# Performance work log

Measured on AMD Instinct MI355X. Metric: run time of the kernel, lower is better.

The kernel has to match this reference:

```python
import jax, jax.numpy as jnp
import numpy as np

B, N = 16, 512          # graphs, nodes per graph (equal-size dynamic batch)
IN, HID, OUT, K = 256, 128, 256, 16  # hidden = in_dim // red_factor
EPS = 1e-5


def setup_inputs() -> dict:
    key = jax.random.key(0)
    ks = jax.random.split(key, 12)
    def lin(k, fi, fo):
        return jax.random.normal(k, (fi, fo), jnp.float32) / np.sqrt(fi).astype(np.float32)
    return {
        "obj_encs": jax.random.normal(ks[0], (B * N, IN), jnp.float32),
        "n_nodes": jnp.full((B,), N, dtype=jnp.int32),
        # self-graph-attention params (in -> hidden), with residual projection
        "Wq": lin(ks[1], IN, HID), "bq": jnp.zeros((HID,), jnp.float32),
        "Wk": lin(ks[2], IN, HID), "bk": jnp.zeros((HID,), jnp.float32),
        "Wv": lin(ks[3], IN, HID), "bv": jnp.zeros((HID,), jnp.float32),
        "Wr": lin(ks[4], IN, HID), "br": jnp.zeros((HID,), jnp.float32),
        # EdgeConv (local+global => 2*HID input features)
        "Wc": lin(ks[5], 2 * HID, OUT), "bc": jnp.zeros((OUT,), jnp.float32),
        # LayerNorm affine
        "ln_scale": jnp.ones((OUT,), jnp.float32),
        "ln_bias": jnp.zeros((OUT,), jnp.float32),
    }


def _forward(obj_encs, n_nodes, Wq, bq, Wk, bk, Wv, bv, Wr, br, Wc, bc, ln_scale, ln_bias):
    # dynamic batching: equal-size graphs per n_nodes -> reshape [B, N, IN]
    x = obj_encs.reshape(B, N, IN)

    # --- SelfGraphAttentionLinear (per-graph dot-product attention, residual) ---
    q = x @ Wq + bq                      # [B, N, HID]
    kk = x @ Wk + bk
    v = x @ Wv + bv
    attn = jax.nn.softmax(jnp.einsum('bnd,bmd->bnm', q, kk) / np.sqrt(HID).astype(np.float32), axis=-1)
    h = jnp.einsum('bnm,bmd->bnd', attn, v) + (x @ Wr + br)  # residual projection

    # --- GraphConv: kNN (euclidean) within each graph ---
    sq = jnp.sum(h * h, axis=-1)                             # [B, N]
    dist = sq[:, :, None] + sq[:, None, :] - 2.0 * jnp.einsum('bnd,bmd->bnm', h, h)
    _, idx = jax.lax.top_k(-dist, K)                         # [B, N, K] (self included)

    nb = jax.vmap(lambda hb, ib: hb[ib])(h, idx)             # [B, N, K, HID]
    hc = h[:, :, None, :]                                    # [B, N, 1, HID]
    # features='local+global': [x_i, x_j - x_i]
    e = jnp.concatenate([jnp.broadcast_to(hc, nb.shape), nb - hc], axis=-1)  # [B,N,K,2H]

    y = jnp.einsum('bnkf,fo->bnko', e, Wc) + bc              # [B, N, K, OUT]
    y = jnp.max(y, axis=2)                                   # reduction='max' over k

    mu = jnp.mean(y, axis=-1, keepdims=True)
    var = jnp.mean((y - mu) ** 2, axis=-1, keepdims=True)
    y = (y - mu) / jnp.sqrt(var + EPS) * ln_scale + ln_bias  # LayerNorm
    return jax.nn.selu(y).reshape(B * N, OUT)


def reference(obj_encs, n_nodes, Wq, bq, Wk, bk, Wv, bv, Wr, br, Wc, bc, ln_scale, ln_bias):
    return _forward(obj_encs, n_nodes, Wq, bq, Wk, bk, Wv, bv, Wr, br, Wc, bc, ln_scale, ln_bias)
```

## Files before the change

### kernel.cpp

```cpp
#include <hip/hip_runtime.h>
#include <math.h>

#define NB   16
#define NN   512
#define FIN  256
#define HID  128
#define FOUT 256
#define TOPK 16
#define ROWS (NB*NN)
#define LN_EPS 1e-5f

#define BK   32
#define LDK  40
#define NTHR 256

typedef __attribute__((ext_vector_type(8)))  short  bf16x8;
typedef __attribute__((ext_vector_type(4)))  float  f32x4;
typedef __attribute__((ext_vector_type(8)))  unsigned short u16x8;

#define MFMA3(d, ah, al, bh, bl)                                              \
    d = __builtin_amdgcn_mfma_f32_16x16x32_bf16(ah, bh, d, 0, 0, 0);          \
    d = __builtin_amdgcn_mfma_f32_16x16x32_bf16(ah, bl, d, 0, 0, 0);          \
    d = __builtin_amdgcn_mfma_f32_16x16x32_bf16(al, bh, d, 0, 0, 0);

__device__ __forceinline__ ushort f2bf_rn(float x) {
    uint u = __float_as_uint(x);
    u += 0x7fff + ((u >> 16) & 1);
    return (ushort)(u >> 16);
}
__device__ __forceinline__ float bf2f(ushort h) {
    return __uint_as_float(((uint)h) << 16);
}
__device__ __forceinline__ void split2(float x, ushort& hi, ushort& lo) {
    hi = f2bf_rn(x);
    lo = f2bf_rn(x - bf2f(hi));
}

__device__ __forceinline__ void stage_rows64f(ushort (*Dh)[LDK], ushort (*Dl)[LDK],
                                              const float* __restrict__ src,
                                              int rstride, int tid)
{
    const int r = tid >> 2, seg = (tid & 3) * 8;
    const float* p = src + (size_t)r * rstride + seg;
    #pragma unroll
    for (int i = 0; i < 2; i++) {
        const float4 q = *(const float4*)(p + 4*i);
        ushort h0,l0,h1,l1,h2,l2,h3,l3;
        split2(q.x,h0,l0); split2(q.y,h1,l1);
        split2(q.z,h2,l2); split2(q.w,h3,l3);
        *(ushort4*)&Dh[r][seg + 4*i] = make_ushort4(h0,h1,h2,h3);
        *(ushort4*)&Dl[r][seg + 4*i] = make_ushort4(l0,l1,l2,l3);
    }
}

__device__ __forceinline__ void stage_cols64f(ushort (*Dh)[LDK], ushort (*Dl)[LDK],
                                              const float* __restrict__ src,
                                              int ldn, int tid)
{
    const int n = tid & 63, kh = (tid >> 6) * 8;
    const float* p = src + (size_t)kh * ldn + n;
    ushort hh[8], ll[8];
    #pragma unroll
    for (int i = 0; i < 8; i++) split2(p[(size_t)i * ldn], hh[i], ll[i]);
    *(ushort4*)&Dh[n][kh]     = make_ushort4(hh[0],hh[1],hh[2],hh[3]);
    *(ushort4*)&Dh[n][kh + 4] = make_ushort4(hh[4],hh[5],hh[6],hh[7]);
    *(ushort4*)&Dl[n][kh]     = make_ushort4(ll[0],ll[1],ll[2],ll[3]);
    *(ushort4*)&Dl[n][kh + 4] = make_ushort4(ll[4],ll[5],ll[6],ll[7]);
}

__device__ __forceinline__ void stage_u(ushort (*Ds)[LDK], const ushort* __restrict__ src,
                                        int rstride, int tid)
{
    const int r = tid >> 2, seg = (tid & 3) * 8;
    *(u16x8*)&Ds[r][seg] = *(const u16x8*)(src + (size_t)r * rstride + seg);
}

__device__ __forceinline__ void mma_step64(const ushort (*Ah)[LDK], const ushort (*Al)[LDK],
                                           const ushort (*Bh)[LDK], const ushort (*Bl)[LDK],
                                           f32x4 acc[2][2], int wr, int wc, int lane)
{
    const int q8 = (lane >> 4) * 8, m = lane & 15;
    bf16x8 ah[2], al[2], bh[2], bl[2];
    #pragma unroll
    for (int i = 0; i < 2; i++) {
        ah[i] = *(const bf16x8*)&Ah[wr + 16*i + m][q8];
        al[i] = *(const bf16x8*)&Al[wr + 16*i + m][q8];
        bh[i] = *(const bf16x8*)&Bh[wc + 16*i + m][q8];
        bl[i] = *(const bf16x8*)&Bl[wc + 16*i + m][q8];
    }
    #pragma unroll
    for (int i = 0; i < 2; i++)
        #pragma unroll
        for (int j = 0; j < 2; j++) {
            MFMA3(acc[i][j], ah[i], al[i], bh[j], bl[j]);
        }
}

struct Params {
    const float *X, *Wq, *bq, *Wk, *bk, *Wv, *bv, *Wr, *br, *Wc, *bc, *lns, *lnb;
    float *out;
    float *Rbuf, *SQ, *AB, *D, *Opart, *Mpart, *Lpart;
    ushort *Yh, *Yl, *Vth, *Vtl, *Hh, *Hl;
};

__device__ void phaseA(const Params& P, ushort* SMEM, int blk, int nblk)
{
    ushort (*Ah)[LDK] = (ushort(*)[LDK])(SMEM);
    ushort (*Al)[LDK] = (ushort(*)[LDK])(SMEM + 2560);
    ushort (*Bh)[LDK] = (ushort(*)[LDK])(SMEM + 5120);
    ushort (*Bl)[LDK] = (ushort(*)[LDK])(SMEM + 7680);
    float* fbuf = (float*)SMEM;

    const int tid = threadIdx.x, lane = tid & 63, w = tid >> 6;
    const int wr = (w >> 1) * 32, wc = (w & 1) * 32;
    const int m = lane & 15, q4 = (lane >> 4) * 4;

    for (int job = blk; job < 1024; job += nblk) {
        const int ct = job >> 7, br0 = (job & 127) * 64;
        const int widx = ct >> 1, ch = (ct & 1) * 64;
        const float* W    = widx==0 ? P.Wq : widx==1 ? P.Wk : widx==2 ? P.Wv : P.Wr;
        const float* bias = widx==0 ? P.bq : widx==1 ? P.bk : widx==2 ? P.bv : P.br;
        __syncthreads();
        f32x4 acc[2][2];
        #pragma unroll
        for (int i = 0; i < 2; i++)
            #pragma unroll
            for (int j = 0; j < 2; j++) acc[i][j] = (f32x4){0.f,0.f,0.f,0.f};

        for (int k0 = 0; k0 < FIN; k0 += BK) {
            stage_rows64f(Ah, Al, P.X + (size_t)br0 * FIN + k0, FIN, tid);
            stage_cols64f(Bh, Bl, W + (size_t)k0 * HID + ch, HID, tid);
            __syncthreads();
            mma_step64(Ah, Al, Bh, Bl, acc, wr, wc, lane);
            __syncthreads();
        }
        #pragma unroll
        for (int i = 0; i < 2; i++)
            #pragma unroll
            for (int reg = 0; reg < 4; reg++) {
                const int r = wr + 16*i + q4 + reg;
                #pragma unroll
                for (int j = 0; j < 2; j++) {
                    const int c = wc + 16*j + m;
                    fbuf[r*65 + c] = acc[i][j][reg] + bias[ch + c];
                }
            }
        __syncthreads();

        if (ct < 4) {
            const int r = tid >> 2, cs = (tid & 3) * 16;
            u16x8 vh0, vh1, vl0, vl1;
            #pragma unroll
            for (int t = 0; t < 8; t++) {
                ushort hh, ll;
                split2(fbuf[r*65 + cs + t], hh, ll);     vh0[t]=hh; vl0[t]=ll;
                split2(fbuf[r*65 + cs + 8 + t], hh, ll); vh1[t]=hh; vl1[t]=ll;
            }
            const size_t o = (size_t)(br0 + r) * 256 + ct*64 + cs;
            *(u16x8*)&P.Yh[o]   = vh0; *(u16x8*)&P.Yh[o+8] = vh1;
            *(u16x8*)&P.Yl[o]   = vl0; *(u16x8*)&P.Yl[o+8] = vl1;
        } else if (ct < 6) {
            const int cl = tid >> 2, rs = (tid & 3) * 16;
            const int b = br0 >> 9, nb = br0 & 511;
            const int cglob = (ct - 4) * 64 + cl;
            u16x8 vh0, vh1, vl0, vl1;
            #pragma unroll
            for (int t = 0; t < 8; t++) {
                ushort hh, ll;
                split2(fbuf[(rs+t)*65 + cl], hh, ll);   vh0[t]=hh; vl0[t]=ll;
                split2(fbuf[(rs+8+t)*65 + cl], hh, ll); vh1[t]=hh; vl1[t]=ll;
            }
            const size_t o = ((size_t)b*128 + cglob) * 512 + nb + rs;
            *(u16x8*)&P.Vth[o]   = vh0; *(u16x8*)&P.Vth[o+8] = vh1;
            *(u16x8*)&P.Vtl[o]   = vl0; *(u16x8*)&P.Vtl[o+8] = vl1;
        } else {
            const int r = tid >> 2, cs = (tid & 3) * 16;
            float* dst = P.Rbuf + (size_t)(br0 + r) * 128 + (ct - 6)*64 + cs;
            #pragma unroll
            for (int t = 0; t < 16; t += 4) {
                float4 q;
                q.x = fbuf[r*65+cs+t];   q.y = fbuf[r*65+cs+t+1];
                q.z = fbuf[r*65+cs+t+2]; q.w = fbuf[r*65+cs+t+3];
                *(float4*)(dst + t) = q;
            }
        }
    }
}

__device__ void phaseB(const Params& P, ushort* SMEM, int blk, int nblk)
{
    ushort (*P0h)[LDK] = (ushort(*)[LDK])(SMEM);
    ushort (*P0l)[LDK] = (ushort(*)[LDK])(SMEM + 2560);
    ushort (*Bh)[LDK]  = (ushort(*)[LDK])(SMEM + 5120);
    ushort (*Bl)[LDK]  = (ushort(*)[LDK])(SMEM + 7680);

    const int tid = threadIdx.x, lane = tid & 63, w = tid >> 6;
    const int L = lane & 15, quad = lane >> 4;
    const float scale = 0.08838834764831845f;

    for (int job = blk; job < 1024; job += nblk) {
        const int b = job >> 6, rest = job & 63;
        const int n0 = (rest >> 3) * 64, mc = rest & 7, m0 = mc * 64;
        const int grow0 = b*NN + n0 + w*16;

        bf16x8 qh[4], ql[4];
        #pragma unroll
        for (int s = 0; s < 4; s++) {
            const size_t qo = (size_t)(grow0 + L) * 256 + s*32 + quad*8;
            qh[s] = *(const bf16x8*)(P.Yh + qo);
            ql[s] = *(const bf16x8*)(P.Yl + qo);
        }

        f32x4 Sf[4];
        #pragma unroll
        for (int j = 0; j < 4; j++) Sf[j] = (f32x4){0.f,0.f,0.f,0.f};

        for (int s = 0; s < 4; s++) {
            __syncthreads();
            {
                const int r = tid >> 2, seg = (tid & 3) * 8;
                const size_t o = (size_t)(b*NN + m0 + r) * 256 + 128 + s*32 + seg;
                *(u16x8*)&Bh[r][seg] = *(const u16x8*)(P.Yh + o);
                *(u16x8*)&Bl[r][seg] = *(const u16x8*)(P.Yl + o);
            }
            __syncthreads();
            #pragma unroll
            for (int j = 0; j < 4; j++) {
                bf16x8 kh = *(const bf16x8*)&Bh[16*j + L][quad*8];
                bf16x8 kl = *(const bf16x8*)&Bl[16*j + L][quad*8];
                MFMA3(Sf[j], qh[s], ql[s], kh, kl);
            }
        }
        #pragma unroll
        for (int j = 0; j < 4; j++)
            #pragma unroll
            for (int r = 0; r < 4; r++) Sf[j][r] *= scale;

        float mx[4], ls[4];
        #pragma unroll
        for (int r = 0; r < 4; r++) {
            float v = fmaxf(fmaxf(Sf[0][r], Sf[1][r]), fmaxf(Sf[2][r], Sf[3][r]));
            v = fmaxf(v, __shfl_xor(v, 1));
            v = fmaxf(v, __shfl_xor(v, 2));
            v = fmaxf(v, __shfl_xor(v, 4));
            v = fmaxf(v, __shfl_xor(v, 8));
            mx[r] = v; ls[r] = 0.f;
        }

        __syncthreads();

        #pragma unroll
        for (int j = 0; j < 4; j++)
            #pragma unroll
            for (int r = 0; r < 4; r++) {
                const float p = __expf(Sf[j][r] - mx[r]);
                ls[r] += p;
                const int row = w*16 + quad*4 + r, cc = (16*j + (lane & 15)) & 31;
                ushort hh, ll; split2(p, hh, ll);
                if (j < 2) { P0h[row][cc] = hh; P0l[row][cc] = ll; }
                else       { Bh[row][cc]  = hh; Bl[row][cc]  = ll; }
            }
        #pragma unroll
        for (int r = 0; r < 4; r++) {
            float v = ls[r];
            v += __shfl_xor(v, 1); v += __shfl_xor(v, 2);
            v += __shfl_xor(v, 4); v += __shfl_xor(v, 8);
            ls[r] = v;
        }

        f32x4 O[8];
        #pragma unroll
        for (int j = 0; j < 8; j++) O[j] = (f32x4){0.f,0.f,0.f,0.f};
        #pragma unroll
        for (int s2 = 0; s2 < 2; s2++) {
            bf16x8 ph = s2 ? *(const bf16x8*)&Bh[w*16 + L][quad*8]
                           : *(const bf16x8*)&P0h[w*16 + L][quad*8];
            bf16x8 pl = s2 ? *(const bf16x8*)&Bl[w*16 + L][quad*8]
                           : *(const bf16x8*)&P0l[w*16 + L][quad*8];
            #pragma unroll
            for (int j = 0; j < 8; j++) {
                const size_t vo = ((size_t)(b*128 + 16*j + L)) * 512 + m0 + s2*32 + quad*8;
                bf16x8 vh = *(const bf16x8*)(P.Vth + vo);
                bf16x8 vl = *(const bf16x8*)(P.Vtl + vo);
                MFMA3(O[j], ph, pl, vh, vl);
            }
        }

        #pragma unroll
        for (int j = 0; j < 8; j++)
            #pragma unroll
            for (int reg = 0; reg < 4; reg++) {
                const int grow = grow0 + quad*4 + reg;
                P.Opart[((size_t)mc*ROWS + grow)*128 + 16*j + L] = O[j][reg];
            }
        if (L == 0) {
            #pragma unroll
            for (int reg = 0; reg < 4; reg++) {
                const int grow = grow0 + quad*4 + reg;
                P.Mpart[(size_t)mc*ROWS + grow] = mx[reg];
                P.Lpart[(size_t)mc*ROWS + grow] = ls[reg];
            }
        }
    }
}

__device__ void phaseC(const Params& P, int blk, int nblk)
{
    const int lane = threadIdx.x & 63, w = threadIdx.x >> 6;
    for (int row = blk*4 + w; row < ROWS; row += nblk*4) {
        float mp[8], M = -INFINITY;
        #pragma unroll
        for (int p = 0; p < 8; p++) {
            mp[p] = P.Mpart[(size_t)p*ROWS + row];
            M = fmaxf(M, mp[p]);
        }
        float Ls = 0.f, o0 = 0.f, o1 = 0.f;
        #pragma unroll
        for (int p = 0; p < 8; p++) {
            const float e = __expf(mp[p] - M);
            Ls += e * P.Lpart[(size_t)p*ROWS + row];
            const float* op = P.Opart + ((size_t)p*ROWS + row)*128;
            o0 += e * op[lane];
            o1 += e * op[lane + 64];
        }
        const float invl = 1.0f / Ls;
        const float h0 = o0*invl + P.Rbuf[(size_t)row*128 + lane];
        const float h1 = o1*invl + P.Rbuf[(size_t)row*128 + lane + 64];
        ushort hh, ll;
        split2(h0, hh, ll); P.Hh[(size_t)row*128 + lane] = hh;      P.Hl[(size_t)row*128 + lane] = ll;
        split2(h1, hh, ll); P.Hh[(size_t)row*128 + lane + 64] = hh; P.Hl[(size_t)row*128 + lane + 64] = ll;
        float s = h0*h0 + h1*h1;
        #pragma unroll
        for (int off = 1; off < 64; off <<= 1) s += __shfl_xor(s, off);
        if (lane == 0) P.SQ[row] = s;
    }
}

__device__ void phaseD(const Params& P, ushort* SMEM, int blk, int nblk)
{
    ushort (*Ah)[LDK] = (ushort(*)[LDK])(SMEM);
    ushort (*Al)[LDK] = (ushort(*)[LDK])(SMEM + 2560);
    ushort (*Bh)[LDK] = (ushort(*)[LDK])(SMEM + 5120);
    ushort (*Bl)[LDK] = (ushort(*)[LDK])(SMEM + 7680);

    const int tid = threadIdx.x, lane = tid & 63, w = tid >> 6;
    const int wr = (w >> 1) * 32, wc = (w & 1) * 32;
    const int m = lane & 15, q4 = (lane >> 4) * 4;

    for (int job = blk; job < 2048; job += nblk) {
        __syncthreads();
        f32x4 acc[2][2];
        #pragma unroll
        for (int i = 0; i < 2; i++)
            #pragma unroll
            for (int j = 0; j < 2; j++) acc[i][j] = (f32x4){0.f,0.f,0.f,0.f};

        if (job < 1024) {
            const int ct = job >> 7, br0 = (job & 127) * 64;
            const bool bhalf = ct >= 4;
            const int c0 = (ct & 3) * 64;
            for (int k0 = 0; k0 < HID; k0 += BK) {
                stage_u(Ah, P.Hh + (size_t)br0 * 128 + k0, 128, tid);
                stage_u(Al, P.Hl + (size_t)br0 * 128 + k0, 128, tid);
                {
                    const int n = tid & 63, kh2 = (tid >> 6) * 8;
                    ushort hh[8], llv[8];
                    #pragma unroll
                    for (int i = 0; i < 8; i++) {
                        const int k = k0 + kh2 + i;
                        const float bot = P.Wc[(size_t)(HID + k) * FOUT + c0 + n];
                        const float val = bhalf ? bot
                                                : (P.Wc[(size_t)k * FOUT + c0 + n] - bot);
                        split2(val, hh[i], llv[i]);
                    }
                    *(ushort4*)&Bh[n][kh2]     = make_ushort4(hh[0],hh[1],hh[2],hh[3]);
                    *(ushort4*)&Bh[n][kh2 + 4] = make_ushort4(hh[4],hh[5],hh[6],hh[7]);
                    *(ushort4*)&Bl[n][kh2]     = make_ushort4(llv[0],llv[1],llv[2],llv[3]);
                    *(ushort4*)&Bl[n][kh2 + 4] = make_ushort4(llv[4],llv[5],llv[6],llv[7]);
                }
                __syncthreads();
                mma_step64(Ah, Al, Bh, Bl, acc, wr, wc, lane);
                __syncthreads();
            }
            #pragma unroll
            for (int i = 0; i < 2; i++)
                #pragma unroll
                for (int reg = 0; reg < 4; reg++) {
                    const int grow = br0 + wr + 16*i + q4 + reg;
                    #pragma unroll
                    for (int j = 0; j < 2; j++) {
                        const int c = wc + 16*j + m;
                        const float add = bhalf ? 0.0f : P.bc[c0 + c];
                        P.AB[(size_t)grow * 512 + ct*64 + c] = acc[i][j][reg] + add;
                    }
                }
        } else {
            const int t = job - 1024;
            const int b = t >> 6, rest = t & 63;
            const int m0 = (rest >> 3) * 64, n0 = (rest & 7) * 64;
            for (int k0 = 0; k0 < HID; k0 += BK) {
                stage_u(Ah, P.Hh + (size_t)(b*NN + n0) * 128 + k0, 128, tid);
                stage_u(Al, P.Hl + (size_t)(b*NN + n0) * 128 + k0, 128, tid);
                stage_u(Bh, P.Hh + (size_t)(b*NN + m0) * 128 + k0, 128, tid);
                stage_u(Bl, P.Hl + (size_t)(b*NN + m0) * 128 + k0, 128, tid);
                __syncthreads();
                mma_step64(Ah, Al, Bh, Bl, acc, wr, wc, lane);
                __syncthreads();
            }
            const int gb = b * NN;
            float* Db = P.D + (size_t)b * NN * NN;
            float sqm[2];
            #pragma unroll
            for (int j = 0; j < 2; j++) sqm[j] = P.SQ[gb + m0 + wc + 16*j + m];
            #pragma unroll
            for (int i = 0; i < 2; i++)
                #pragma unroll
                for (int reg = 0; reg < 4; reg++) {
                    const int n = n0 + wr + 16*i + q4 + reg;
                    const float sqn = P.SQ[gb + n];
                    #pragma unroll
                    for (int j = 0; j < 2; j++)
                        Db[(size_t)n * NN + m0 + wc + 16*j + m]
                            = sqn + sqm[j] - 2.0f * acc[i][j][reg];
                }
        }
    }
}

__device__ void phaseE(const Params& P, int blk, int nblk)
{
    const int lane = threadIdx.x & 63, w = threadIdx.x >> 6;
    for (int row = blk*4 + w; row < ROWS; row += nblk*4) {
        const int gb0 = row & ~(NN - 1);
        const float* drow = P.D + (size_t)row * NN;
        const float4 dq0 = ((const float4*)drow)[lane];
        const float4 dq1 = ((const float4*)drow)[64 + lane];
        float v[8] = {dq0.x, dq0.y, dq0.z, dq0.w, dq1.x, dq1.y, dq1.z, dq1.w};

        const float lsc0 = P.lns[lane],       lbi0 = P.lnb[lane];
        const float lsc1 = P.lns[lane + 64],  lbi1 = P.lnb[lane + 64];
        const float lsc2 = P.lns[lane + 128], lbi2 = P.lnb[lane + 128];
        const float lsc3 = P.lns[lane + 192], lbi3 = P.lnb[lane + 192];
        const float* arow = P.AB + (size_t)row * 512;
        const float a0 = arow[lane], a1 = arow[lane + 64],
                    a2 = arow[lane + 128], a3 = arow[lane + 192];

        float bm0 = -INFINITY, bm1 = -INFINITY, bm2 = -INFINITY, bm3 = -INFINITY;

        for (int it = 0; it < TOPK; it++) {
            float bestv = v[0]; int bestm = 4*lane;
            #pragma unroll
            for (int j = 1; j < 8; j++) {
                const int mm = (j >> 2)*256 + 4*lane + (j & 3);
                if (v[j] < bestv) { bestv = v[j]; bestm = mm; }
            }
            #pragma unroll
            for (int off = 1; off < 64; off <<= 1) {
                const float ov = __shfl_xor(bestv, off);
                const int   om = __shfl_xor(bestm, off);
                if (ov < bestv || (ov == bestv && om < bestm)) { bestv = ov; bestm = om; }
            }
            const float* brow = P.AB + (size_t)(gb0 + bestm) * 512 + 256;
            bm0 = fmaxf(bm0, brow[lane]);
            bm1 = fmaxf(bm1, brow[lane + 64]);
            bm2 = fmaxf(bm2, brow[lane + 128]);
            bm3 = fmaxf(bm3, brow[lane + 192]);
            if (((bestm >> 2) & 63) == lane) {
                const int jj = ((bestm >> 8) << 2) | (bestm & 3);
                #pragma unroll
                for (int j = 0; j < 8; j++) if (j == jj) v[j] = INFINITY;
            }
        }

        float y0 = a0 + bm0, y1 = a1 + bm1, y2 = a2 + bm2, y3 = a3 + bm3;
        float s = y0 + y1 + y2 + y3;
        #pragma unroll
        for (int off = 1; off < 64; off <<= 1) s += __shfl_xor(s, off);
        const float mu = s * (1.0f/256.0f);
        const float d0 = y0 - mu, d1 = y1 - mu, d2 = y2 - mu, d3 = y3 - mu;
        float s2 = d0*d0 + d1*d1 + d2*d2 + d3*d3;
        #pragma unroll
        for (int off = 1; off < 64; off <<= 1) s2 += __shfl_xor(s2, off);
        const float var = s2 * (1.0f/256.0f);
        const float rstd = rsqrtf(var + LN_EPS);

        const float lam = 1.0507009873554805f, alpha = 1.6732632423543772f;
        float* orow = P.out + (size_t)row * FOUT;
        { const float z = d0*rstd*lsc0 + lbi0; orow[lane]       = z > 0.f ? lam*z : lam*alpha*expm1f(z); }
        { const float z = d1*rstd*lsc1 + lbi1; orow[lane + 64]  = z > 0.f ? lam*z : lam*alpha*expm1f(z); }
        { const float z = d2*rstd*lsc2 + lbi2; orow[lane + 128] = z > 0.f ? lam*z : lam*alpha*expm1f(z); }
        { const float z = d3*rstd*lsc3 + lbi3; orow[lane + 192] = z > 0.f ? lam*z : lam*alpha*expm1f(z); }
    }
}

__global__ __launch_bounds__(NTHR, 2) void k_pA(Params P) {
    __shared__ ushort SMEM[4*64*LDK];
    phaseA(P, SMEM, blockIdx.x, gridDim.x);
}
__global__ __launch_bounds__(NTHR, 2) void k_pB(Params P) {
    __shared__ ushort SMEM[4*64*LDK];
    phaseB(P, SMEM, blockIdx.x, gridDim.x);
}
__global__ __launch_bounds__(NTHR, 2) void k_pC(Params P) { phaseC(P, blockIdx.x, gridDim.x); }
__global__ __launch_bounds__(NTHR, 2) void k_pD(Params P) {
    __shared__ ushort SMEM[4*64*LDK];
    phaseD(P, SMEM, blockIdx.x, gridDim.x);
}
__global__ __launch_bounds__(NTHR, 2) void k_pE(Params P) { phaseE(P, blockIdx.x, gridDim.x); }

extern "C" void kernel_launch(void* const* d_in, const int* in_sizes, int n_in,
                              void* d_out, int out_size, void* d_ws, size_t ws_size,
                              hipStream_t stream)
{
    (void)in_sizes; (void)n_in; (void)out_size; (void)ws_size;

    char* cur = (char*)d_ws;
    auto alloc = [&](size_t bytes) { char* p = cur; cur += (bytes + 255) & ~size_t(255); return p; };

    Params P;
    P.X   = (const float*)d_in[0];
    P.Wq  = (const float*)d_in[2];
    P.bq  = (const float*)d_in[3];
    P.Wk  = (const float*)d_in[4];
    P.bk  = (const float*)d_in[5];
    P.Wv  = (const float*)d_in[6];
    P.bv  = (const float*)d_in[7];
    P.Wr  = (const float*)d_in[8];
    P.br  = (const float*)d_in[9];
    P.Wc  = (const float*)d_in[10];
    P.bc  = (const float*)d_in[11];
    P.lns = (const float*)d_in[12];
    P.lnb = (const float*)d_in[13];
    P.out = (float*)d_out;

    P.D     = (float*)alloc((size_t)NB*NN*NN*4);
    P.AB    = (float*)alloc((size_t)ROWS*512*4);
    P.Opart = (float*)alloc((size_t)8*ROWS*128*4);
    P.Mpart = (float*)alloc((size_t)8*ROWS*4);
    P.Lpart = (float*)alloc((size_t)8*ROWS*4);
    P.Rbuf  = (float*)alloc((size_t)ROWS*128*4);
    P.SQ    = (float*)alloc((size_t)ROWS*4);
    P.Yh    = (ushort*)alloc((size_t)ROWS*256*2);
    P.Yl    = (ushort*)alloc((size_t)ROWS*256*2);
    P.Vth   = (ushort*)alloc((size_t)NB*128*512*2);
    P.Vtl   = (ushort*)alloc((size_t)NB*128*512*2);
    P.Hh    = (ushort*)alloc((size_t)ROWS*128*2);
    P.Hl    = (ushort*)alloc((size_t)ROWS*128*2);

    k_pA<<<1024, NTHR, 0, stream>>>(P);
    k_pB<<<1024, NTHR, 0, stream>>>(P);
    k_pC<<<2048, NTHR, 0, stream>>>(P);
    k_pD<<<2048, NTHR, 0, stream>>>(P);
    k_pE<<<2048, NTHR, 0, stream>>>(P);
}
```

Baseline: 184.7 us.

## Pre-split inputs and weights into bf16 hi/lo in a prep kernel

Adds a prep kernel that converts X once into bf16 hi/lo arrays and pre-transposes and splits the QKVR and EdgeConv weights, including a folded (Wtop - Wbot) form, plus concatenated biases. Phase A then stages pre-split bf16 tiles with vector loads instead of splitting floats and doing strided column loads on every tile, and each phase becomes a one-job-per-block kernel. This removes the split work that was repeated across the column tiles of the projection GEMM. The cost is an extra launch and extra global traffic to write and re-read the bf16 copies of X.

```diff
diff --git a/kernel.cpp b/kernel.cpp
--- a/kernel.cpp
+++ b/kernel.cpp
@@ -36,38 +36,6 @@
     lo = f2bf_rn(x - bf2f(hi));
 }
 
-__device__ __forceinline__ void stage_rows64f(ushort (*Dh)[LDK], ushort (*Dl)[LDK],
-                                              const float* __restrict__ src,
-                                              int rstride, int tid)
-{
-    const int r = tid >> 2, seg = (tid & 3) * 8;
-    const float* p = src + (size_t)r * rstride + seg;
-    #pragma unroll
-    for (int i = 0; i < 2; i++) {
-        const float4 q = *(const float4*)(p + 4*i);
-        ushort h0,l0,h1,l1,h2,l2,h3,l3;
-        split2(q.x,h0,l0); split2(q.y,h1,l1);
-        split2(q.z,h2,l2); split2(q.w,h3,l3);
-        *(ushort4*)&Dh[r][seg + 4*i] = make_ushort4(h0,h1,h2,h3);
-        *(ushort4*)&Dl[r][seg + 4*i] = make_ushort4(l0,l1,l2,l3);
-    }
-}
-
-__device__ __forceinline__ void stage_cols64f(ushort (*Dh)[LDK], ushort (*Dl)[LDK],
-                                              const float* __restrict__ src,
-                                              int ldn, int tid)
-{
-    const int n = tid & 63, kh = (tid >> 6) * 8;
-    const float* p = src + (size_t)kh * ldn + n;
-    ushort hh[8], ll[8];
-    #pragma unroll
-    for (int i = 0; i < 8; i++) split2(p[(size_t)i * ldn], hh[i], ll[i]);
-    *(ushort4*)&Dh[n][kh]     = make_ushort4(hh[0],hh[1],hh[2],hh[3]);
-    *(ushort4*)&Dh[n][kh + 4] = make_ushort4(hh[4],hh[5],hh[6],hh[7]);
-    *(ushort4*)&Dl[n][kh]     = make_ushort4(ll[0],ll[1],ll[2],ll[3]);
-    *(ushort4*)&Dl[n][kh + 4] = make_ushort4(ll[4],ll[5],ll[6],ll[7]);
-}
-
 __device__ __forceinline__ void stage_u(ushort (*Ds)[LDK], const ushort* __restrict__ src,
                                         int rstride, int tid)
 {
@@ -99,12 +67,110 @@
 struct Params {
     const float *X, *Wq, *bq, *Wk, *bk, *Wv, *bv, *Wr, *br, *Wc, *bc, *lns, *lnb;
     float *out;
-    float *Rbuf, *SQ, *AB, *D, *Opart, *Mpart, *Lpart;
-    ushort *Yh, *Yl, *Vth, *Vtl, *Hh, *Hl;
+    float *Rbuf, *SQ, *AB, *D, *Opart, *Mpart, *Lpart, *bcat, *bcab;
+    ushort *Xh, *Xl, *Yh, *Yl, *Vth, *Vtl, *Hh, *Hl, *Wth, *Wtl, *Wcth, *Wctl;
 };
 
-__device__ void phaseA(const Params& P, ushort* SMEM, int blk, int nblk)
-{
+__global__ __launch_bounds__(NTHR) void k_prep(Params P)
+{
+    const int blk = blockIdx.x, tid = threadIdx.x;
+    __shared__ float fb[64][65];
+
+    if (blk >= 17) {
+        const size_t base = ((size_t)(blk - 17) * 256 + tid) * 8;
+        const float4 a = *(const float4*)(P.X + base);
+        const float4 b = *(const float4*)(P.X + base + 4);
+        u16x8 vh, vl; ushort hh, ll;
+        split2(a.x,hh,ll); vh[0]=hh; vl[0]=ll;
+        split2(a.y,hh,ll); vh[1]=hh; vl[1]=ll;
+        split2(a.z,hh,ll); vh[2]=hh; vl[2]=ll;
+        split2(a.w,hh,ll); vh[3]=hh; vl[3]=ll;
+        split2(b.x,hh,ll); vh[4]=hh; vl[4]=ll;
+        split2(b.y,hh,ll); vh[5]=hh; vl[5]=ll;
+        split2(b.z,hh,ll); vh[6]=hh; vl[6]=ll;
+        split2(b.w,hh,ll); vh[7]=hh; vl[7]=ll;
+        *(u16x8*)(P.Xh + base) = vh;
+        *(u16x8*)(P.Xl + base) = vl;
+        return;
+    }
+
+    if (blk < 8) {
+        const int n0 = blk * 64;
+        const int widx = n0 >> 7;
+        const float* W = widx==0 ? P.Wq : widx==1 ? P.Wk : widx==2 ? P.Wv : P.Wr;
+        const int cbase = n0 & 127;
+        for (int kt = 0; kt < 4; kt++) {
+            const int k0 = kt * 64;
+            __syncthreads();
+            {
+                const int kk = tid >> 2, cs = (tid & 3) * 16;
+                #pragma unroll
+                for (int t = 0; t < 16; t += 4) {
+                    const float4 q = *(const float4*)&W[(size_t)(k0+kk)*HID + cbase + cs + t];
+                    fb[kk][cs+t]=q.x; fb[kk][cs+t+1]=q.y; fb[kk][cs+t+2]=q.z; fb[kk][cs+t+3]=q.w;
+                }
+            }
+            __syncthreads();
+            {
+                const int c = tid >> 2, ks = (tid & 3) * 16;
+                u16x8 vh0, vh1, vl0, vl1;
+                #pragma unroll
+                for (int t = 0; t < 8; t++) {
+                    ushort hh, ll;
+                    split2(fb[ks+t][c], hh, ll);   vh0[t]=hh; vl0[t]=ll;
+                    split2(fb[ks+8+t][c], hh, ll); vh1[t]=hh; vl1[t]=ll;
+                }
+                *(u16x8*)&P.Wth[(size_t)(n0+c)*256 + k0 + ks]     = vh0;
+                *(u16x8*)&P.Wth[(size_t)(n0+c)*256 + k0 + ks + 8] = vh1;
+                *(u16x8*)&P.Wtl[(size_t)(n0+c)*256 + k0 + ks]     = vl0;
+                *(u16x8*)&P.Wtl[(size_t)(n0+c)*256 + k0 + ks + 8] = vl1;
+            }
+        }
+    } else if (blk < 16) {
+        const int n0 = (blk - 8) * 64;
+        const bool ahalf = n0 < 256;
+        const int cbase = n0 & 255;
+        for (int kt = 0; kt < 2; kt++) {
+            const int k0 = kt * 64;
+            __syncthreads();
+            {
+                const int kk = tid >> 2, cs = (tid & 3) * 16;
+                #pragma unroll
+                for (int t = 0; t < 16; t++) {
+                    const float bot = P.Wc[(size_t)(HID + k0 + kk)*FOUT + cbase + cs + t];
+                    float val = bot;
+                    if (ahalf) val = P.Wc[(size_t)(k0 + kk)*FOUT + cbase + cs + t] - bot;
+                    fb[kk][cs+t] = val;
+                }
+            }
+            __syncthreads();
+            {
+                const int c = tid >> 2, ks = (tid & 3) * 16;
+                u16x8 vh0, vh1, vl0, vl1;
+                #pragma unroll
+                for (int t = 0; t < 8; t++) {
+                    ushort hh, ll;
+                    split2(fb[ks+t][c], hh, ll);   vh0[t]=hh; vl0[t]=ll;
+                    split2(fb[ks+8+t][c], hh, ll); vh1[t]=hh; vl1[t]=ll;
+                }
+                *(u16x8*)&P.Wcth[(size_t)(n0+c)*128 + k0 + ks]     = vh0;
+                *(u16x8*)&P.Wcth[(size_t)(n0+c)*128 + k0 + ks + 8] = vh1;
+                *(u16x8*)&P.Wctl[(size_t)(n0+c)*128 + k0 + ks]     = vl0;
+                *(u16x8*)&P.Wctl[(size_t)(n0+c)*128 + k0 + ks + 8] = vl1;
+            }
+        }
+    } else {
+        for (int i = tid; i < 512; i += 256) {
+            const int w = i >> 7, c = i & 127;
+            P.bcat[i] = w==0 ? P.bq[c] : w==1 ? P.bk[c] : w==2 ? P.bv[c] : P.br[c];
+            P.bcab[i] = i < 256 ? P.bc[i] : 0.f;
+        }
+    }
+}
+
+__global__ __launch_bounds__(NTHR, 2) void k_pA(Params P)
+{
+    __shared__ ushort SMEM[4*64*LDK];
     ushort (*Ah)[LDK] = (ushort(*)[LDK])(SMEM);
     ushort (*Al)[LDK] = (ushort(*)[LDK])(SMEM + 2560);
     ushort (*Bh)[LDK] = (ushort(*)[LDK])(SMEM + 5120);
@@ -115,80 +181,80 @@
     const int wr = (w >> 1) * 32, wc = (w & 1) * 32;
     const int m = lane & 15, q4 = (lane >> 4) * 4;
 
-    for (int job = blk; job < 1024; job += nblk) {
-        const int ct = job >> 7, br0 = (job & 127) * 64;
-        const int widx = ct >> 1, ch = (ct & 1) * 64;
-        const float* W    = widx==0 ? P.Wq : widx==1 ? P.Wk : widx==2 ? P.Wv : P.Wr;
-        const float* bias = widx==0 ? P.bq : widx==1 ? P.bk : widx==2 ? P.bv : P.br;
+    const int job = blockIdx.x;
+    const int ct = job >> 7, br0 = (job & 127) * 64;
+
+    f32x4 acc[2][2];
+    #pragma unroll
+    for (int i = 0; i < 2; i++)
+        #pragma unroll
+        for (int j = 0; j < 2; j++) acc[i][j] = (f32x4){0.f,0.f,0.f,0.f};
+
+    for (int k0 = 0; k0 < FIN; k0 += BK) {
+        stage_u(Ah, P.Xh + (size_t)br0 * 256 + k0, 256, tid);
+        stage_u(Al, P.Xl + (size_t)br0 * 256 + k0, 256, tid);
+        stage_u(Bh, P.Wth + (size_t)(ct*64) * 256 + k0, 256, tid);
+        stage_u(Bl, P.Wtl + (size_t)(ct*64) * 256 + k0, 256, tid);
         __syncthreads();
-        f32x4 acc[2][2];
-        #pragma unroll
-        for (int i = 0; i < 2; i++)
+        mma_step64(Ah, Al, Bh, Bl, acc, wr, wc, lane);
+        __syncthreads();
+    }
+
+    #pragma unroll
+    for (int i = 0; i < 2; i++)
+        #pragma unroll
+        for (int reg = 0; reg < 4; reg++) {
+            const int r = wr + 16*i + q4 + reg;
             #pragma unroll
-            for (int j = 0; j < 2; j++) acc[i][j] = (f32x4){0.f,0.f,0.f,0.f};
-
-        for (int k0 = 0; k0 < FIN; k0 += BK) {
-            stage_rows64f(Ah, Al, P.X + (size_t)br0 * FIN + k0, FIN, tid);
-            stage_cols64f(Bh, Bl, W + (size_t)k0 * HID + ch, HID, tid);
-            __syncthreads();
-            mma_step64(Ah, Al, Bh, Bl, acc, wr, wc, lane);
-            __syncthreads();
-        }
-        #pragma unroll
-        for (int i = 0; i < 2; i++)
-            #pragma unroll
-            for (int reg = 0; reg < 4; reg++) {
-                const int r = wr + 16*i + q4 + reg;
-                #pragma unroll
-                for (int j = 0; j < 2; j++) {
-                    const int c = wc + 16*j + m;
-                    fbuf[r*65 + c] = acc[i][j][reg] + bias[ch + c];
-                }
-            }
-        __syncthreads();
-
-        if (ct < 4) {
-            const int r = tid >> 2, cs = (tid & 3) * 16;
-            u16x8 vh0, vh1, vl0, vl1;
-            #pragma unroll
-            for (int t = 0; t < 8; t++) {
-                ushort hh, ll;
-                split2(fbuf[r*65 + cs + t], hh, ll);     vh0[t]=hh; vl0[t]=ll;
-                split2(fbuf[r*65 + cs + 8 + t], hh, ll); vh1[t]=hh; vl1[t]=ll;
-            }
-            const size_t o = (size_t)(br0 + r) * 256 + ct*64 + cs;
-            *(u16x8*)&P.Yh[o]   = vh0; *(u16x8*)&P.Yh[o+8] = vh1;
-            *(u16x8*)&P.Yl[o]   = vl0; *(u16x8*)&P.Yl[o+8] = vl1;
-        } else if (ct < 6) {
-            const int cl = tid >> 2, rs = (tid & 3) * 16;
-            const int b = br0 >> 9, nb = br0 & 511;
-            const int cglob = (ct - 4) * 64 + cl;
-            u16x8 vh0, vh1, vl0, vl1;
-            #pragma unroll
-            for (int t = 0; t < 8; t++) {
-                ushort hh, ll;
-                split2(fbuf[(rs+t)*65 + cl], hh, ll);   vh0[t]=hh; vl0[t]=ll;
-                split2(fbuf[(rs+8+t)*65 + cl], hh, ll); vh1[t]=hh; vl1[t]=ll;
-            }
-            const size_t o = ((size_t)b*128 + cglob) * 512 + nb + rs;
-            *(u16x8*)&P.Vth[o]   = vh0; *(u16x8*)&P.Vth[o+8] = vh1;
-            *(u16x8*)&P.Vtl[o]   = vl0; *(u16x8*)&P.Vtl[o+8] = vl1;
-        } else {
-            const int r = tid >> 2, cs = (tid & 3) * 16;
-            float* dst = P.Rbuf + (size_t)(br0 + r) * 128 + (ct - 6)*64 + cs;
-            #pragma unroll
-            for (int t = 0; t < 16; t += 4) {
-                float4 q;
-                q.x = fbuf[r*65+cs+t];   q.y = fbuf[r*65+cs+t+1];
-                q.z = fbuf[r*65+cs+t+2]; q.w = fbuf[r*65+cs+t+3];
-                *(float4*)(dst + t) = q;
-            }
-        }
-    }
-}
-
-__device__ void phaseB(const Params& P, ushort* SMEM, int blk, int nblk)
-{
+            for (int j = 0; j < 2; j++) {
+                const int c = wc + 16*j + m;
+                fbuf[r*65 + c] = acc[i][j][reg] + P.bcat[ct*64 + c];
+            }
+        }
+    __syncthreads();
+
+    if (ct < 4) {
+        const int r = tid >> 2, cs = (tid & 3) * 16;
+        u16x8 vh0, vh1, vl0, vl1;
+        #pragma unroll
+        for (int t = 0; t < 8; t++) {
+            ushort hh, ll;
+            split2(fbuf[r*65 + cs + t], hh, ll);     vh0[t]=hh; vl0[t]=ll;
+            split2(fbuf[r*65 + cs + 8 + t], hh, ll); vh1[t]=hh; vl1[t]=ll;
+        }
+        const size_t o = (size_t)(br0 + r) * 256 + ct*64 + cs;
+        *(u16x8*)&P.Yh[o]   = vh0; *(u16x8*)&P.Yh[o+8] = vh1;
+        *(u16x8*)&P.Yl[o]   = vl0; *(u16x8*)&P.Yl[o+8] = vl1;
+    } else if (ct < 6) {
+        const int cl = tid >> 2, rs = (tid & 3) * 16;
+        const int b = br0 >> 9, nb = br0 & 511;
+        const int cglob = (ct - 4) * 64 + cl;
+        u16x8 vh0, vh1, vl0, vl1;
+        #pragma unroll
+        for (int t = 0; t < 8; t++) {
+            ushort hh, ll;
+            split2(fbuf[(rs+t)*65 + cl], hh, ll);   vh0[t]=hh; vl0[t]=ll;
+            split2(fbuf[(rs+8+t)*65 + cl], hh, ll); vh1[t]=hh; vl1[t]=ll;
+        }
+        const size_t o = ((size_t)b*128 + cglob) * 512 + nb + rs;
+        *(u16x8*)&P.Vth[o]   = vh0; *(u16x8*)&P.Vth[o+8] = vh1;
+        *(u16x8*)&P.Vtl[o]   = vl0; *(u16x8*)&P.Vtl[o+8] = vl1;
+    } else {
+        const int r = tid >> 2, cs = (tid & 3) * 16;
+        float* dst = P.Rbuf + (size_t)(br0 + r) * 128 + (ct - 6)*64 + cs;
+        #pragma unroll
+        for (int t = 0; t < 16; t += 4) {
+            float4 q;
+            q.x = fbuf[r*65+cs+t];   q.y = fbuf[r*65+cs+t+1];
+            q.z = fbuf[r*65+cs+t+2]; q.w = fbuf[r*65+cs+t+3];
+            *(float4*)(dst + t) = q;
+        }
+    }
+}
+
+__global__ __launch_bounds__(NTHR, 2) void k_pB(Params P)
+{
+    __shared__ ushort SMEM[4*64*LDK];
     ushort (*P0h)[LDK] = (ushort(*)[LDK])(SMEM);
     ushort (*P0l)[LDK] = (ushort(*)[LDK])(SMEM + 2560);
     ushort (*Bh)[LDK]  = (ushort(*)[LDK])(SMEM + 5120);
@@ -198,146 +264,145 @@
     const int L = lane & 15, quad = lane >> 4;
     const float scale = 0.08838834764831845f;
 
-    for (int job = blk; job < 1024; job += nblk) {
-        const int b = job >> 6, rest = job & 63;
-        const int n0 = (rest >> 3) * 64, mc = rest & 7, m0 = mc * 64;
-        const int grow0 = b*NN + n0 + w*16;
-
-        bf16x8 qh[4], ql[4];
-        #pragma unroll
-        for (int s = 0; s < 4; s++) {
-            const size_t qo = (size_t)(grow0 + L) * 256 + s*32 + quad*8;
-            qh[s] = *(const bf16x8*)(P.Yh + qo);
-            ql[s] = *(const bf16x8*)(P.Yl + qo);
-        }
-
-        f32x4 Sf[4];
-        #pragma unroll
-        for (int j = 0; j < 4; j++) Sf[j] = (f32x4){0.f,0.f,0.f,0.f};
-
-        for (int s = 0; s < 4; s++) {
-            __syncthreads();
-            {
-                const int r = tid >> 2, seg = (tid & 3) * 8;
-                const size_t o = (size_t)(b*NN + m0 + r) * 256 + 128 + s*32 + seg;
-                *(u16x8*)&Bh[r][seg] = *(const u16x8*)(P.Yh + o);
-                *(u16x8*)&Bl[r][seg] = *(const u16x8*)(P.Yl + o);
-            }
-            __syncthreads();
-            #pragma unroll
-            for (int j = 0; j < 4; j++) {
-                bf16x8 kh = *(const bf16x8*)&Bh[16*j + L][quad*8];
-                bf16x8 kl = *(const bf16x8*)&Bl[16*j + L][quad*8];
-                MFMA3(Sf[j], qh[s], ql[s], kh, kl);
-            }
-        }
-        #pragma unroll
-        for (int j = 0; j < 4; j++)
-            #pragma unroll
-            for (int r = 0; r < 4; r++) Sf[j][r] *= scale;
-
-        float mx[4], ls[4];
+    const int job = blockIdx.x;
+    const int b = job >> 6, rest = job & 63;
+    const int n0 = (rest >> 3) * 64, mc = rest & 7, m0 = mc * 64;
+    const int grow0 = b*NN + n0 + w*16;
+
+    bf16x8 qh[4], ql[4];
+    #pragma unroll
+    for (int s = 0; s < 4; s++) {
+        const size_t qo = (size_t)(grow0 + L) * 256 + s*32 + quad*8;
+        qh[s] = *(const bf16x8*)(P.Yh + qo);
+        ql[s] = *(const bf16x8*)(P.Yl + qo);
+    }
+
+    f32x4 Sf[4];
+    #pragma unroll
+    for (int j = 0; j < 4; j++) Sf[j] = (f32x4){0.f,0.f,0.f,0.f};
+
+    for (int s = 0; s < 4; s++) {
+        __syncthreads();
+        {
+            const int r = tid >> 2, seg = (tid & 3) * 8;
+            const size_t o = (size_t)(b*NN + m0 + r) * 256 + 128 + s*32 + seg;
+            *(u16x8*)&Bh[r][seg] = *(const u16x8*)(P.Yh + o);
+            *(u16x8*)&Bl[r][seg] = *(const u16x8*)(P.Yl + o);
+        }
+        __syncthreads();
+        #pragma unroll
+        for (int j = 0; j < 4; j++) {
+            bf16x8 kh = *(const bf16x8*)&Bh[16*j + L][quad*8];
+            bf16x8 kl = *(const bf16x8*)&Bl[16*j + L][quad*8];
+            MFMA3(Sf[j], qh[s], ql[s], kh, kl);
+        }
+    }
+    #pragma unroll
+    for (int j = 0; j < 4; j++)
+        #pragma unroll
+        for (int r = 0; r < 4; r++) Sf[j][r] *= scale;
+
+    float mx[4], ls[4];
+    #pragma unroll
+    for (int r = 0; r < 4; r++) {
+        float v = fmaxf(fmaxf(Sf[0][r], Sf[1][r]), fmaxf(Sf[2][r], Sf[3][r]));
+        v = fmaxf(v, __shfl_xor(v, 1));
+        v = fmaxf(v, __shfl_xor(v, 2));
+        v = fmaxf(v, __shfl_xor(v, 4));
+        v = fmaxf(v, __shfl_xor(v, 8));
+        mx[r] = v; ls[r] = 0.f;
+    }
+
+    __syncthreads();
+
+    #pragma unroll
+    for (int j = 0; j < 4; j++)
         #pragma unroll
         for (int r = 0; r < 4; r++) {
-            float v = fmaxf(fmaxf(Sf[0][r], Sf[1][r]), fmaxf(Sf[2][r], Sf[3][r]));
-            v = fmaxf(v, __shfl_xor(v, 1));
-            v = fmaxf(v, __shfl_xor(v, 2));
-            v = fmaxf(v, __shfl_xor(v, 4));
-            v = fmaxf(v, __shfl_xor(v, 8));
-            mx[r] = v; ls[r] = 0.f;
-        }
-
-        __syncthreads();
-
-        #pragma unroll
-        for (int j = 0; j < 4; j++)
-            #pragma unroll
-            for (int r = 0; r < 4; r++) {
-                const float p = __expf(Sf[j][r] - mx[r]);
-                ls[r] += p;
-                const int row = w*16 + quad*4 + r, cc = (16*j + (lane & 15)) & 31;
-                ushort hh, ll; split2(p, hh, ll);
-                if (j < 2) { P0h[row][cc] = hh; P0l[row][cc] = ll; }
-                else       { Bh[row][cc]  = hh; Bl[row][cc]  = ll; }
-            }
-        #pragma unroll
-        for (int r = 0; r < 4; r++) {
-            float v = ls[r];
-            v += __shfl_xor(v, 1); v += __shfl_xor(v, 2);
-            v += __shfl_xor(v, 4); v += __shfl_xor(v, 8);
-            ls[r] = v;
-        }
-
-        f32x4 O[8];
-        #pragma unroll
-        for (int j = 0; j < 8; j++) O[j] = (f32x4){0.f,0.f,0.f,0.f};
-        #pragma unroll
-        for (int s2 = 0; s2 < 2; s2++) {
-            bf16x8 ph = s2 ? *(const bf16x8*)&Bh[w*16 + L][quad*8]
-                           : *(const bf16x8*)&P0h[w*16 + L][quad*8];
-            bf16x8 pl = s2 ? *(const bf16x8*)&Bl[w*16 + L][quad*8]
-                           : *(const bf16x8*)&P0l[w*16 + L][quad*8];
-            #pragma unroll
-            for (int j = 0; j < 8; j++) {
-                const size_t vo = ((size_t)(b*128 + 16*j + L)) * 512 + m0 + s2*32 + quad*8;
-                bf16x8 vh = *(const bf16x8*)(P.Vth + vo);
-                bf16x8 vl = *(const bf16x8*)(P.Vtl + vo);
-                MFMA3(O[j], ph, pl, vh, vl);
-            }
-        }
-
-        #pragma unroll
-        for (int j = 0; j < 8; j++)
-            #pragma unroll
-            for (int reg = 0; reg < 4; reg++) {
-                const int grow = grow0 + quad*4 + reg;
-                P.Opart[((size_t)mc*ROWS + grow)*128 + 16*j + L] = O[j][reg];
-            }
-        if (L == 0) {
-            #pragma unroll
-            for (int reg = 0; reg < 4; reg++) {
-                const int grow = grow0 + quad*4 + reg;
-                P.Mpart[(size_t)mc*ROWS + grow] = mx[reg];
-                P.Lpart[(size_t)mc*ROWS + grow] = ls[reg];
-            }
-        }
-    }
-}
-
-__device__ void phaseC(const Params& P, int blk, int nblk)
+            const float p = __expf(Sf[j][r] - mx[r]);
+            ls[r] += p;
+            const int row = w*16 + quad*4 + r, cc = (16*j + L) & 31;
+            ushort hh, ll; split2(p, hh, ll);
+            if (j < 2) { P0h[row][cc] = hh; P0l[row][cc] = ll; }
+            else       { Bh[row][cc]  = hh; Bl[row][cc]  = ll; }
+        }
+    #pragma unroll
+    for (int r = 0; r < 4; r++) {
+        float v = ls[r];
+        v += __shfl_xor(v, 1); v += __shfl_xor(v, 2);
+        v += __shfl_xor(v, 4); v += __shfl_xor(v, 8);
+        ls[r] = v;
+    }
+
+    f32x4 O[8];
+    #pragma unroll
+    for (int j = 0; j < 8; j++) O[j] = (f32x4){0.f,0.f,0.f,0.f};
+    #pragma unroll
+    for (int s2 = 0; s2 < 2; s2++) {
+        bf16x8 ph = s2 ? *(const bf16x8*)&Bh[w*16 + L][quad*8]
+                       : *(const bf16x8*)&P0h[w*16 + L][quad*8];
+        bf16x8 pl = s2 ? *(const bf16x8*)&Bl[w*16 + L][quad*8]
+                       : *(const bf16x8*)&P0l[w*16 + L][quad*8];
+        #pragma unroll
+        for (int j = 0; j < 8; j++) {
+            const size_t vo = ((size_t)(b*128 + 16*j + L)) * 512 + m0 + s2*32 + quad*8;
+            bf16x8 vh = *(const bf16x8*)(P.Vth + vo);
+            bf16x8 vl = *(const bf16x8*)(P.Vtl + vo);
+            MFMA3(O[j], ph, pl, vh, vl);
+        }
+    }
+
+    #pragma unroll
+    for (int j = 0; j < 8; j++)
+        #pragma unroll
+        for (int reg = 0; reg < 4; reg++) {
+            const int grow = grow0 + quad*4 + reg;
+            P.Opart[((size_t)mc*ROWS + grow)*128 + 16*j + L] = O[j][reg];
+        }
+    if (L == 0) {
+        #pragma unroll
+        for (int reg = 0; reg < 4; reg++) {
+            const int grow = grow0 + quad*4 + reg;
+            P.Mpart[(size_t)mc*ROWS + grow] = mx[reg];
+            P.Lpart[(size_t)mc*ROWS + grow] = ls[reg];
+        }
+    }
+}
+
+__global__ __launch_bounds__(NTHR, 2) void k_pC(Params P)
 {
     const int lane = threadIdx.x & 63, w = threadIdx.x >> 6;
-    for (int row = blk*4 + w; row < ROWS; row += nblk*4) {
-        float mp[8], M = -INFINITY;
-        #pragma unroll
-        for (int p = 0; p < 8; p++) {
-            mp[p] = P.Mpart[(size_t)p*ROWS + row];
-            M = fmaxf(M, mp[p]);
-        }
-        float Ls = 0.f, o0 = 0.f, o1 = 0.f;
-        #pragma unroll
-        for (int p = 0; p < 8; p++) {
-            const float e = __expf(mp[p] - M);
-            Ls += e * P.Lpart[(size_t)p*ROWS + row];
-            const float* op = P.Opart + ((size_t)p*ROWS + row)*128;
-            o0 += e * op[lane];
-            o1 += e * op[lane + 64];
-        }
-        const float invl = 1.0f / Ls;
-        const float h0 = o0*invl + P.Rbuf[(size_t)row*128 + lane];
-        const float h1 = o1*invl + P.Rbuf[(size_t)row*128 + lane + 64];
-        ushort hh, ll;
-        split2(h0, hh, ll); P.Hh[(size_t)row*128 + lane] = hh;      P.Hl[(size_t)row*128 + lane] = ll;
-        split2(h1, hh, ll); P.Hh[(size_t)row*128 + lane + 64] = hh; P.Hl[(size_t)row*128 + lane + 64] = ll;
-        float s = h0*h0 + h1*h1;
-        #pragma unroll
-        for (int off = 1; off < 64; off <<= 1) s += __shfl_xor(s, off);
-        if (lane == 0) P.SQ[row] = s;
-    }
-}
-
-__device__ void phaseD(const Params& P, ushort* SMEM, int blk, int nblk)
-{
+    const int row = blockIdx.x * 4 + w;
+    float mp[8], M = -INFINITY;
+    #pragma unroll
+    for (int p = 0; p < 8; p++) {
+        mp[p] = P.Mpart[(size_t)p*ROWS + row];
+        M = fmaxf(M, mp[p]);
+    }
+    float Ls = 0.f, o0 = 0.f, o1 = 0.f;
+    #pragma unroll
+    for (int p = 0; p < 8; p++) {
+        const float e = __expf(mp[p] - M);
+        Ls += e * P.Lpart[(size_t)p*ROWS + row];
+        const float* op = P.Opart + ((size_t)p*ROWS + row)*128;
+        o0 += e * op[lane];
+        o1 += e * op[lane + 64];
+    }
+    const float invl = 1.0f / Ls;
+    const float h0 = o0*invl + P.Rbuf[(size_t)row*128 + lane];
+    const float h1 = o1*invl + P.Rbuf[(size_t)row*128 + lane + 64];
+    ushort hh, ll;
+    split2(h0, hh, ll); P.Hh[(size_t)row*128 + lane] = hh;      P.Hl[(size_t)row*128 + lane] = ll;
+    split2(h1, hh, ll); P.Hh[(size_t)row*128 + lane + 64] = hh; P.Hl[(size_t)row*128 + lane + 64] = ll;
+    float s = h0*h0 + h1*h1;
+    #pragma unroll
+    for (int off = 1; off < 64; off <<= 1) s += __shfl_xor(s, off);
+    if (lane == 0) P.SQ[row] = s;
+}
+
+__global__ __launch_bounds__(NTHR, 2) void k_pD(Params P)
+{
+    __shared__ ushort SMEM[4*64*LDK];
     ushort (*Ah)[LDK] = (ushort(*)[LDK])(SMEM);
     ushort (*Al)[LDK] = (ushort(*)[LDK])(SMEM + 2560);
     ushort (*Bh)[LDK] = (ushort(*)[LDK])(SMEM + 5120);
@@ -346,167 +411,132 @@
     const int tid = threadIdx.x, lane = tid & 63, w = tid >> 6;
     const int wr = (w >> 1) * 32, wc = (w & 1) * 32;
     const int m = lane & 15, q4 = (lane >> 4) * 4;
-
-    for (int job = blk; job < 2048; job += nblk) {
-        __syncthreads();
-        f32x4 acc[2][2];
+    const int job = blockIdx.x;
+
+    f32x4 acc[2][2];
+    #pragma unroll
+    for (int i = 0; i < 2; i++)
+        #pragma unroll
+        for (int j = 0; j < 2; j++) acc[i][j] = (f32x4){0.f,0.f,0.f,0.f};
+
+    if (job < 1024) {
+        const int ct = job >> 7, br0 = (job & 127) * 64;
+        for (int k0 = 0; k0 < HID; k0 += BK) {
+            stage_u(Ah, P.Hh + (size_t)br0 * 128 + k0, 128, tid);
+            stage_u(Al, P.Hl + (size_t)br0 * 128 + k0, 128, tid);
+            stage_u(Bh, P.Wcth + (size_t)(ct*64) * 128 + k0, 128, tid);
+            stage_u(Bl, P.Wctl + (size_t)(ct*64) * 128 + k0, 128, tid);
+            __syncthreads();
+            mma_step64(Ah, Al, Bh, Bl, acc, wr, wc, lane);
+            __syncthreads();
+        }
         #pragma unroll
         for (int i = 0; i < 2; i++)
             #pragma unroll
-            for (int j = 0; j < 2; j++) acc[i][j] = (f32x4){0.f,0.f,0.f,0.f};
-
-        if (job < 1024) {
-            const int ct = job >> 7, br0 = (job & 127) * 64;
-            const bool bhalf = ct >= 4;
-            const int c0 = (ct & 3) * 64;
-            for (int k0 = 0; k0 < HID; k0 += BK) {
-                stage_u(Ah, P.Hh + (size_t)br0 * 128 + k0, 128, tid);
-                stage_u(Al, P.Hl + (size_t)br0 * 128 + k0, 128, tid);
-                {
-                    const int n = tid & 63, kh2 = (tid >> 6) * 8;
-                    ushort hh[8], llv[8];
-                    #pragma unroll
-                    for (int i = 0; i < 8; i++) {
-                        const int k = k0 + kh2 + i;
-                        const float bot = P.Wc[(size_t)(HID + k) * FOUT + c0 + n];
-                        const float val = bhalf ? bot
-                                                : (P.Wc[(size_t)k * FOUT + c0 + n] - bot);
-                        split2(val, hh[i], llv[i]);
-                    }
-                    *(ushort4*)&Bh[n][kh2]     = make_ushort4(hh[0],hh[1],hh[2],hh[3]);
-                    *(ushort4*)&Bh[n][kh2 + 4] = make_ushort4(hh[4],hh[5],hh[6],hh[7]);
-                    *(ushort4*)&Bl[n][kh2]     = make_ushort4(llv[0],llv[1],llv[2],llv[3]);
-                    *(ushort4*)&Bl[n][kh2 + 4] = make_ushort4(llv[4],llv[5],llv[6],llv[7]);
+            for (int reg = 0; reg < 4; reg++) {
+                const int grow = br0 + wr + 16*i + q4 + reg;
+                #pragma unroll
+                for (int j = 0; j < 2; j++) {
+                    const int c = wc + 16*j + m;
+                    P.AB[(size_t)grow * 512 + ct*64 + c] = acc[i][j][reg] + P.bcab[ct*64 + c];
                 }
-                __syncthreads();
-                mma_step64(Ah, Al, Bh, Bl, acc, wr, wc, lane);
-                __syncthreads();
-            }
+            }
+    } else {
+        const int t = job - 1024;
+        const int b = t >> 6, rest = t & 63;
+        const int m0 = (rest >> 3) * 64, n0 = (rest & 7) * 64;
+        for (int k0 = 0; k0 < HID; k0 += BK) {
+            stage_u(Ah, P.Hh + (size_t)(b*NN + n0) * 128 + k0, 128, tid);
+            stage_u(Al, P.Hl + (size_t)(b*NN + n0) * 128 + k0, 128, tid);
+            stage_u(Bh, P.Hh + (size_t)(b*NN + m0) * 128 + k0, 128, tid);
+            stage_u(Bl, P.Hl + (size_t)(b*NN + m0) * 128 + k0, 128, tid);
+            __syncthreads();
+            mma_step64(Ah, Al, Bh, Bl, acc, wr, wc, lane);
+            __syncthreads();
+        }
+        const int gb = b * NN;
+        float* Db = P.D + (size_t)b * NN * NN;
+        float sqm[2];
+        #pragma unroll
+        for (int j = 0; j < 2; j++) sqm[j] = P.SQ[gb + m0 + wc + 16*j + m];
+        #pragma unroll
+        for (int i = 0; i < 2; i++)
             #pragma unroll
-            for (int i = 0; i < 2; i++)
+            for (int reg = 0; reg < 4; reg++) {
+                const int n = n0 + wr + 16*i + q4 + reg;
+                const float sqn = P.SQ[gb + n];
                 #pragma unroll
-                for (int reg = 0; reg < 4; reg++) {
-                    const int grow = br0 + wr + 16*i + q4 + reg;
-                    #pragma unroll
-                    for (int j = 0; j < 2; j++) {
-                        const int c = wc + 16*j + m;
-                        const float add = bhalf ? 0.0f : P.bc[c0 + c];
-                        P.AB[(size_t)grow * 512 + ct*64 + c] = acc[i][j][reg] + add;
-                    }
-                }
-        } else {
-            const int t = job - 1024;
-            const int b = t >> 6, rest = t & 63;
-            const int m0 = (rest >> 3) * 64, n0 = (rest & 7) * 64;
-            for (int k0 = 0; k0 < HID; k0 += BK) {
-                stage_u(Ah, P.Hh + (size_t)(b*NN + n0) * 128 + k0, 128, tid);
-                stage_u(Al, P.Hl + (size_t)(b*NN + n0) * 128 + k0, 128, tid);
-                stage_u(Bh, P.Hh + (size_t)(b*NN + m0) * 128 + k0, 128, tid);
-                stage_u(Bl, P.Hl + (size_t)(b*NN + m0) * 128 + k0, 128, tid);
-                __syncthreads();
-                mma_step64(Ah, Al, Bh, Bl, acc, wr, wc, lane);
-                __syncthreads();
-            }
-            const int gb = b * NN;
-            float* Db = P.D + (size_t)b * NN * NN;
-            float sqm[2];
+                for (int j = 0; j < 2; j++)
+                    Db[(size_t)n * NN + m0 + wc + 16*j + m]
+                        = sqn + sqm[j] - 2.0f * acc[i][j][reg];
+            }
+    }
+}
+
+__global__ __launch_bounds__(NTHR, 2) void k_pE(Params P)
+{
+    const int lane = threadIdx.x & 63, w = threadIdx.x >> 6;
+    const int row = blockIdx.x * 4 + w;
+    const int gb0 = row & ~(NN - 1);
+    const float* drow = P.D + (size_t)row * NN;
+    const float4 dq0 = ((const float4*)drow)[lane];
+    const float4 dq1 = ((const float4*)drow)[64 + lane];
+    float v[8] = {dq0.x, dq0.y, dq0.z, dq0.w, dq1.x, dq1.y, dq1.z, dq1.w};
+
+    const float lsc0 = P.lns[lane],       lbi0 = P.lnb[lane];
+    const float lsc1 = P.lns[lane + 64],  lbi1 = P.lnb[lane + 64];
+    const float lsc2 = P.lns[lane + 128], lbi2 = P.lnb[lane + 128];
+    const float lsc3 = P.lns[lane + 192], lbi3 = P.lnb[lane + 192];
+    const float* arow = P.AB + (size_t)row * 512;
+    const float a0 = arow[lane], a1 = arow[lane + 64],
+                a2 = arow[lane + 128], a3 = arow[lane + 192];
+
+    float bm0 = -INFINITY, bm1 = -INFINITY, bm2 = -INFINITY, bm3 = -INFINITY;
+
+    for (int it = 0; it < TOPK; it++) {
+        float bestv = v[0]; int bestm = 4*lane;
+        #pragma unroll
+        for (int j = 1; j < 8; j++) {
+            const int mm = (j >> 2)*256 + 4*lane + (j & 3);
+            if (v[j] < bestv) { bestv = v[j]; bestm = mm; }
+        }
+        #pragma unroll
+        for (int off = 1; off < 64; off <<= 1) {
+            const float ov = __shfl_xor(bestv, off);
+            const int   om = __shfl_xor(bestm, off);
+            if (ov < bestv || (ov == bestv && om < bestm)) { bestv = ov; bestm = om; }
+        }
+        const float* brow = P.AB + (size_t)(gb0 + bestm) * 512 + 256;
+        bm0 = fmaxf(bm0, brow[lane]);
+        bm1 = fmaxf(bm1, brow[lane + 64]);
+        bm2 = fmaxf(bm2, brow[lane + 128]);
+        bm3 = fmaxf(bm3, brow[lane + 192]);
+        if (((bestm >> 2) & 63) == lane) {
+            const int jj = ((bestm >> 8) << 2) | (bestm & 3);
             #pragma unroll
-            for (int j = 0; j < 2; j++) sqm[j] = P.SQ[gb + m0 + wc + 16*j + m];
-            #pragma unroll
-            for (int i = 0; i < 2; i++)
-                #pragma unroll
-                for (int reg = 0; reg < 4; reg++) {
-                    const int n = n0 + wr + 16*i + q4 + reg;
-                    const float sqn = P.SQ[gb + n];
-                    #pragma unroll
-                    for (int j = 0; j < 2; j++)
-                        Db[(size_t)n * NN + m0 + wc + 16*j + m]
-                            = sqn + sqm[j] - 2.0f * acc[i][j][reg];
-                }
-        }
-    }
-}
-
-__device__ void phaseE(const Params& P, int blk, int nblk)
-{
-    const int lane = threadIdx.x & 63, w = threadIdx.x >> 6;
-    for (int row = blk*4 + w; row < ROWS; row += nblk*4) {
-        const int gb0 = row & ~(NN - 1);
-        const float* drow = P.D + (size_t)row * NN;
-        const float4 dq0 = ((const float4*)drow)[lane];
-        const float4 dq1 = ((const float4*)drow)[64 + lane];
-        float v[8] = {dq0.x, dq0.y, dq0.z, dq0.w, dq1.x, dq1.y, dq1.z, dq1.w};
-
-        const float lsc0 = P.lns[lane],       lbi0 = P.lnb[lane];
-        const float lsc1 = P.lns[lane + 64],  lbi1 = P.lnb[lane + 64];
-        const float lsc2 = P.lns[lane + 128], lbi2 = P.lnb[lane + 128];
-        const float lsc3 = P.lns[lane + 192], lbi3 = P.lnb[lane + 192];
-        const float* arow = P.AB + (size_t)row * 512;
-        const float a0 = arow[lane], a1 = arow[lane + 64],
-                    a2 = arow[lane + 128], a3 = arow[lane + 192];
-
-        float bm0 = -INFINITY, bm1 = -INFINITY, bm2 = -INFINITY, bm3 = -INFINITY;
-
-        for (int it = 0; it < TOPK; it++) {
-            float bestv = v[0]; int bestm = 4*lane;
-            #pragma unroll
-            for (int j = 1; j < 8; j++) {
-                const int mm = (j >> 2)*256 + 4*lane + (j & 3);
-                if (v[j] < bestv) { bestv = v[j]; bestm = mm; }
-            }
-            #pragma unroll
-            for (int off = 1; off < 64; off <<= 1) {
-                const float ov = __shfl_xor(bestv, off);
-                const int   om = __shfl_xor(bestm, off);
-                if (ov < bestv || (ov == bestv && om < bestm)) { bestv = ov; bestm = om; }
-            }
-            const float* brow = P.AB + (size_t)(gb0 + bestm) * 512 + 256;
-            bm0 = fmaxf(bm0, brow[lane]);
-            bm1 = fmaxf(bm1, brow[lane + 64]);
-            bm2 = fmaxf(bm2, brow[lane + 128]);
-            bm3 = fmaxf(bm3, brow[lane + 192]);
-            if (((bestm >> 2) & 63) == lane) {
-                const int jj = ((bestm >> 8) << 2) | (bestm & 3);
-                #pragma unroll
-                for (int j = 0; j < 8; j++) if (j == jj) v[j] = INFINITY;
-            }
-        }
-
-        float y0 = a0 + bm0, y1 = a1 + bm1, y2 = a2 + bm2, y3 = a3 + bm3;
-        float s = y0 + y1 + y2 + y3;
-        #pragma unroll
-        for (int off = 1; off < 64; off <<= 1) s += __shfl_xor(s, off);
-        const float mu = s * (1.0f/256.0f);
-        const float d0 = y0 - mu, d1 = y1 - mu, d2 = y2 - mu, d3 = y3 - mu;
-        float s2 = d0*d0 + d1*d1 + d2*d2 + d3*d3;
-        #pragma unroll
-        for (int off = 1; off < 64; off <<= 1) s2 += __shfl_xor(s2, off);
-        const float var = s2 * (1.0f/256.0f);
-        const float rstd = rsqrtf(var + LN_EPS);
-
-        const float lam = 1.0507009873554805f, alpha = 1.6732632423543772f;
-        float* orow = P.out + (size_t)row * FOUT;
-        { const float z = d0*rstd*lsc0 + lbi0; orow[lane]       = z > 0.f ? lam*z : lam*alpha*expm1f(z); }
-        { const float z = d1*rstd*lsc1 + lbi1; orow[lane + 64]  = z > 0.f ? lam*z : lam*alpha*expm1f(z); }
-        { const float z = d2*rstd*lsc2 + lbi2; orow[lane + 128] = z > 0.f ? lam*z : lam*alpha*expm1f(z); }
-        { const float z = d3*rstd*lsc3 + lbi3; orow[lane + 192] = z > 0.f ? lam*z : lam*alpha*expm1f(z); }
-    }
-}
-
-__global__ __launch_bounds__(NTHR, 2) void k_pA(Params P) {
-    __shared__ ushort SMEM[4*64*LDK];
-    phaseA(P, SMEM, blockIdx.x, gridDim.x);
-}
-__global__ __launch_bounds__(NTHR, 2) void k_pB(Params P) {
-    __shared__ ushort SMEM[4*64*LDK];
-    phaseB(P, SMEM, blockIdx.x, gridDim.x);
-}
-__global__ __launch_bounds__(NTHR, 2) void k_pC(Params P) { phaseC(P, blockIdx.x, gridDim.x); }
-__global__ __launch_bounds__(NTHR, 2) void k_pD(Params P) {
-    __shared__ ushort SMEM[4*64*LDK];
-    phaseD(P, SMEM, blockIdx.x, gridDim.x);
-}
-__global__ __launch_bounds__(NTHR, 2) void k_pE(Params P) { phaseE(P, blockIdx.x, gridDim.x); }
+            for (int j = 0; j < 8; j++) if (j == jj) v[j] = INFINITY;
+        }
+    }
+
+    float y0 = a0 + bm0, y1 = a1 + bm1, y2 = a2 + bm2, y3 = a3 + bm3;
+    float s = y0 + y1 + y2 + y3;
+    #pragma unroll
+    for (int off = 1; off < 64; off <<= 1) s += __shfl_xor(s, off);
+    const float mu = s * (1.0f/256.0f);
+    const float d0 = y0 - mu, d1 = y1 - mu, d2 = y2 - mu, d3 = y3 - mu;
+    float s2 = d0*d0 + d1*d1 + d2*d2 + d3*d3;
+    #pragma unroll
+    for (int off = 1; off < 64; off <<= 1) s2 += __shfl_xor(s2, off);
+    const float var = s2 * (1.0f/256.0f);
+    const float rstd = rsqrtf(var + LN_EPS);
+
+    const float lam = 1.0507009873554805f, alpha = 1.6732632423543772f;
+    float* orow = P.out + (size_t)row * FOUT;
+    { const float z = d0*rstd*lsc0 + lbi0; orow[lane]       = z > 0.f ? lam*z : lam*alpha*expm1f(z); }
+    { const float z = d1*rstd*lsc1 + lbi1; orow[lane + 64]  = z > 0.f ? lam*z : lam*alpha*expm1f(z); }
+    { const float z = d2*rstd*lsc2 + lbi2; orow[lane + 128] = z > 0.f ? lam*z : lam*alpha*expm1f(z); }
+    { const float z = d3*rstd*lsc3 + lbi3; orow[lane + 192] = z > 0.f ? lam*z : lam*alpha*expm1f(z); }
+}
 
 extern "C" void kernel_launch(void* const* d_in, const int* in_sizes, int n_in,
                               void* d_out, int out_size, void* d_ws, size_t ws_size,
@@ -540,16 +570,25 @@
     P.Lpart = (float*)alloc((size_t)8*ROWS*4);
     P.Rbuf  = (float*)alloc((size_t)ROWS*128*4);
     P.SQ    = (float*)alloc((size_t)ROWS*4);
+    P.bcat  = (float*)alloc(512*4);
+    P.bcab  = (float*)alloc(512*4);
+    P.Xh    = (ushort*)alloc((size_t)ROWS*256*2);
+    P.Xl    = (ushort*)alloc((size_t)ROWS*256*2);
     P.Yh    = (ushort*)alloc((size_t)ROWS*256*2);
     P.Yl    = (ushort*)alloc((size_t)ROWS*256*2);
     P.Vth   = (ushort*)alloc((size_t)NB*128*512*2);
     P.Vtl   = (ushort*)alloc((size_t)NB*128*512*2);
     P.Hh    = (ushort*)alloc((size_t)ROWS*128*2);
     P.Hl    = (ushort*)alloc((size_t)ROWS*128*2);
-
-    k_pA<<<1024, NTHR, 0, stream>>>(P);
-    k_pB<<<1024, NTHR, 0, stream>>>(P);
-    k_pC<<<2048, NTHR, 0, stream>>>(P);
-    k_pD<<<2048, NTHR, 0, stream>>>(P);
-    k_pE<<<2048, NTHR, 0, stream>>>(P);
-}
+    P.Wth   = (ushort*)alloc((size_t)512*256*2);
+    P.Wtl   = (ushort*)alloc((size_t)512*256*2);
+    P.Wcth  = (ushort*)alloc((size_t)512*128*2);
+    P.Wctl  = (ushort*)alloc((size_t)512*128*2);
+
+    k_prep<<<17 + 1024, NTHR, 0, stream>>>(P);
+    k_pA  <<<1024,      NTHR, 0, stream>>>(P);
+    k_pB  <<<1024,      NTHR, 0, stream>>>(P);
+    k_pC  <<<2048,      NTHR, 0, stream>>>(P);
+    k_pD  <<<2048,      NTHR, 0, stream>>>(P);
+    k_pE  <<<2048,      NTHR, 0, stream>>>(P);
+}
```

After: 192.9 us. +4.4%, slower.
